# Optimization experiments

Measured on AMD Instinct MI355X. Metric: run time of the kernel, lower is better.

Reference implementation:

```python
import jax, jax.numpy as jnp
import numpy as np
import math

M, DIN, DTGT = 65536, 256, 256   # feature count and feature dims
S, SD_IN, SD_TGT = 64, 256, 256  # num_slots, in_slot_dim, tgt_slot_dim
ITERS = 3
H_IN = 128                        # mlp_in hidden (hardcoded 128 in source)
H_TGT = SD_TGT if SD_TGT > 128 else 128  # mlp_tgt hidden

ARGS = ["inputs", "target", "in_slots", "tgt_slots",
        "ln_in_g", "ln_in_b", "ln_tgt_g", "ln_tgt_b",
        "Wk", "bk", "Wv", "bv", "Wvt", "bvt",
        "ln_slots_g", "ln_slots_b", "Wq", "bq",
        "gru_in_Wih", "gru_in_Whh", "gru_in_bih", "gru_in_bhh",
        "gru_tgt_Wih", "gru_tgt_Whh", "gru_tgt_bih", "gru_tgt_bhh",
        "ln_mi_g", "ln_mi_b", "mi_W1", "mi_b1", "mi_W2", "mi_b2",
        "ln_mt_g", "ln_mt_b", "mt_W1", "mt_b1", "mt_W2", "mt_b2"]


def _ln(x, g, b):
    m = jnp.mean(x, axis=-1, keepdims=True)
    v = jnp.var(x, axis=-1, keepdims=True)
    return (x - m) * jax.lax.rsqrt(v + 1e-5) * g + b


def _gru(x, h, Wih, Whh, bih, bhh):
    # torch.nn.GRUCell semantics; Wih: (D, 3H), Whh: (H, 3H)
    H = h.shape[-1]
    gi = x @ Wih + bih
    gh = h @ Whh + bhh
    r = jax.nn.sigmoid(gi[:, :H] + gh[:, :H])
    z = jax.nn.sigmoid(gi[:, H:2 * H] + gh[:, H:2 * H])
    n = jnp.tanh(gi[:, 2 * H:] + r * gh[:, 2 * H:])
    return (1.0 - z) * n + z * h


def _forward(inputs, target, in_slots, tgt_slots,
             ln_in_g, ln_in_b, ln_tgt_g, ln_tgt_b,
             Wk, bk, Wv, bv, Wvt, bvt,
             ln_slots_g, ln_slots_b, Wq, bq,
             gru_in_Wih, gru_in_Whh, gru_in_bih, gru_in_bhh,
             gru_tgt_Wih, gru_tgt_Whh, gru_tgt_bih, gru_tgt_bhh,
             ln_mi_g, ln_mi_b, mi_W1, mi_b1, mi_W2, mi_b2,
             ln_mt_g, ln_mt_b, mt_W1, mt_b1, mt_W2, mt_b2):
    inputs_norm = _ln(inputs, ln_in_g, ln_in_b)          # [M, DIN]
    in_k = inputs_norm @ Wk + bk                          # [M, SD_IN]
    in_v = inputs_norm @ Wv + bv                          # [M, SD_IN]
    tgt_v = _ln(target, ln_tgt_g, ln_tgt_b) @ Wvt + bvt   # [M, SD_TGT]
    scale = 1.0 / math.sqrt(in_k.shape[1])
    attn = None
    for _ in range(ITERS):
        q = _ln(in_slots, ln_slots_g, ln_slots_b) @ Wq + bq   # [S, SD_IN]
        logits = (q @ in_k.T) * scale                          # [S, M]
        attn = jax.nn.softmax(logits, axis=0)                  # softmax over SLOTS (dim=0)
        in_up = attn @ in_v                                    # [S, SD_IN]
        tgt_up = attn @ tgt_v                                  # [S, SD_TGT]
        in_slots = _gru(in_up, in_slots, gru_in_Wih, gru_in_Whh, gru_in_bih, gru_in_bhh)
        tgt_slots = _gru(tgt_up, tgt_slots, gru_tgt_Wih, gru_tgt_Whh, gru_tgt_bih, gru_tgt_bhh)
        in_slots = in_slots + (jax.nn.relu(_ln(in_slots, ln_mi_g, ln_mi_b) @ mi_W1 + mi_b1) @ mi_W2 + mi_b2)
        tgt_slots = tgt_slots + (jax.nn.relu(_ln(tgt_slots, ln_mt_g, ln_mt_b) @ mt_W1 + mt_b1) @ mt_W2 + mt_b2)
    return (in_slots, tgt_slots, attn)


def setup_inputs() -> dict:
    key = jax.random.key(0)
    ks = iter(jax.random.split(key, 64))
    rn = lambda shape, s=1.0: jax.random.normal(next(ks), shape, dtype=jnp.float32) * s
    w = 0.02
    d = {
        "inputs": rn((M, DIN)),
        "target": rn((M, DTGT)),
        "in_slots": rn((S, SD_IN)),
        "tgt_slots": rn((S, SD_TGT)),
        "ln_in_g": jnp.ones((DIN,)), "ln_in_b": jnp.zeros((DIN,)),
        "ln_tgt_g": jnp.ones((DTGT,)), "ln_tgt_b": jnp.zeros((DTGT,)),
        "Wk": rn((DIN, SD_IN), w), "bk": jnp.zeros((SD_IN,)),
        "Wv": rn((DIN, SD_IN), w), "bv": jnp.zeros((SD_IN,)),
        "Wvt": rn((DTGT, SD_TGT), w), "bvt": jnp.zeros((SD_TGT,)),
        "ln_slots_g": jnp.ones((SD_IN,)), "ln_slots_b": jnp.zeros((SD_IN,)),
        "Wq": rn((SD_IN, SD_IN), w), "bq": jnp.zeros((SD_IN,)),
        "gru_in_Wih": rn((SD_IN, 3 * SD_IN), w), "gru_in_Whh": rn((SD_IN, 3 * SD_IN), w),
        "gru_in_bih": jnp.zeros((3 * SD_IN,)), "gru_in_bhh": jnp.zeros((3 * SD_IN,)),
        "gru_tgt_Wih": rn((SD_TGT, 3 * SD_TGT), w), "gru_tgt_Whh": rn((SD_TGT, 3 * SD_TGT), w),
        "gru_tgt_bih": jnp.zeros((3 * SD_TGT,)), "gru_tgt_bhh": jnp.zeros((3 * SD_TGT,)),
        "ln_mi_g": jnp.ones((SD_IN,)), "ln_mi_b": jnp.zeros((SD_IN,)),
        "mi_W1": rn((SD_IN, H_IN), w), "mi_b1": jnp.zeros((H_IN,)),
        "mi_W2": rn((H_IN, SD_IN), w), "mi_b2": jnp.zeros((SD_IN,)),
        "ln_mt_g": jnp.ones((SD_TGT,)), "ln_mt_b": jnp.zeros((SD_TGT,)),
        "mt_W1": rn((SD_TGT, H_TGT), w), "mt_b1": jnp.zeros((H_TGT,)),
        "mt_W2": rn((H_TGT, SD_TGT), w), "mt_b2": jnp.zeros((SD_TGT,)),
    }
    return {k: d[k] for k in ARGS}


def reference(inputs, target, in_slots, tgt_slots,
              ln_in_g, ln_in_b, ln_tgt_g, ln_tgt_b,
              Wk, bk, Wv, bv, Wvt, bvt,
              ln_slots_g, ln_slots_b, Wq, bq,
              gru_in_Wih, gru_in_Whh, gru_in_bih, gru_in_bhh,
              gru_tgt_Wih, gru_tgt_Whh, gru_tgt_bih, gru_tgt_bhh,
              ln_mi_g, ln_mi_b, mi_W1, mi_b1, mi_W2, mi_b2,
              ln_mt_g, ln_mt_b, mt_W1, mt_b1, mt_W2, mt_b2):
    return _forward(inputs, target, in_slots, tgt_slots,
                    ln_in_g, ln_in_b, ln_tgt_g, ln_tgt_b,
                    Wk, bk, Wv, bv, Wvt, bvt,
                    ln_slots_g, ln_slots_b, Wq, bq,
                    gru_in_Wih, gru_in_Whh, gru_in_bih, gru_in_bhh,
                    gru_tgt_Wih, gru_tgt_Whh, gru_tgt_bih, gru_tgt_bhh,
                    ln_mi_g, ln_mi_b, mi_W1, mi_b1, mi_W2, mi_b2,
                    ln_mt_g, ln_mt_b, mt_W1, mt_b1, mt_W2, mt_b2)
```

## Files before the change

kernel.cpp:

```cpp
#include <hip/hip_runtime.h>
#include <hip/hip_bf16.h>
#include <math.h>

typedef __bf16 bf16_t;
typedef __bf16 bf16x8 __attribute__((ext_vector_type(8)));
typedef __bf16 bf16x4 __attribute__((ext_vector_type(4)));
typedef float f32x4 __attribute__((ext_vector_type(4)));

#define DEVI __device__ __forceinline__

DEVI f32x4 mfma16(bf16x8 a, bf16x8 b, f32x4 c) {
  return __builtin_amdgcn_mfma_f32_16x16x32_bf16(a, b, c, 0, 0, 0);
}
DEVI bf16x8 ld8(const bf16_t* p) { return *reinterpret_cast<const bf16x8*>(p); }

struct WtArgs { const float* s0; const float* s1; const float* s2; const float* s3;
                const float* s4; const float* s5; const float* s6; const float* s7;
                const float* s8; const float* s9; const float* s10; const float* s11; };

__global__ __launch_bounds__(256) void k_wtrans(WtArgs A, bf16_t* __restrict__ wt) {
  constexpr int offs[12] = {0,65536,131072,196608,262144,458752,655360,851968,
                            1048576,1081344,1114112,1179648};
  constexpr int Ks[12]   = {256,256,256,256,256,256,256,256,256,128,256,256};
  constexpr int Ns[12]   = {256,256,256,256,768,768,768,768,128,256,256,256};
  const int m = blockIdx.y;
  const int K = Ks[m], N = Ns[m];
  const int tn = N >> 6;
  const int tile = blockIdx.x;
  if (tile >= (K >> 6) * tn) return;
  const int tk = tile / tn, tc = tile - tk * tn;
  const float* sp;
  switch (m) {
    case 0: sp = A.s0; break; case 1: sp = A.s1; break; case 2: sp = A.s2; break;
    case 3: sp = A.s3; break; case 4: sp = A.s4; break; case 5: sp = A.s5; break;
    case 6: sp = A.s6; break; case 7: sp = A.s7; break; case 8: sp = A.s8; break;
    case 9: sp = A.s9; break; case 10: sp = A.s10; break; default: sp = A.s11; break;
  }
  __shared__ float ts[64][65];
  const int t = threadIdx.x, c = t & 63, rq = t >> 6;
  const int k0 = tk * 64, n0 = tc * 64;
  #pragma unroll
  for (int i = 0; i < 16; ++i) {
    const int r = rq * 16 + i;
    ts[r][c] = sp[(size_t)(k0 + r) * N + n0 + c];
  }
  __syncthreads();
  bf16_t* dst = wt + offs[m];
  #pragma unroll
  for (int i = 0; i < 16; ++i) {
    const int nr = rq * 16 + i;
    dst[(size_t)(n0 + nr) * K + k0 + c] = (bf16_t)ts[c][nr];
  }
}

__global__ __launch_bounds__(256) void k_init(const float* __restrict__ in_slots,
                                              const float* __restrict__ tgt_slots,
                                              float* __restrict__ h_f32,
                                              bf16_t* __restrict__ h_bf) {
  int idx = blockIdx.x * 256 + threadIdx.x;
  int side = idx >> 14, j = idx & 16383;
  float x = (side ? tgt_slots : in_slots)[j];
  h_f32[idx] = x;
  h_bf[idx] = (bf16_t)x;
}

__global__ __launch_bounds__(256) void k_phaseA(
    const float* __restrict__ inputs, const float* __restrict__ target,
    const float* __restrict__ ln_in_g, const float* __restrict__ ln_in_b,
    const float* __restrict__ ln_tgt_g, const float* __restrict__ ln_tgt_b,
    const bf16_t* __restrict__ wkT, const bf16_t* __restrict__ wvT, const bf16_t* __restrict__ wvtT,
    const float* __restrict__ bk, const float* __restrict__ bv, const float* __restrict__ bvt,
    bf16_t* __restrict__ in_k, bf16_t* __restrict__ in_vT, bf16_t* __restrict__ tgt_vT) {
  const int side = blockIdx.y;
  const int m0 = blockIdx.x * 64;
  const int t = threadIdx.x;
  __shared__ __align__(16) bf16_t anorm[64][264];
  __shared__ float gs[256], bs[256];
  {
    const float* g = side ? ln_tgt_g : ln_in_g;
    const float* bb = side ? ln_tgt_b : ln_in_b;
    gs[t] = g[t]; bs[t] = bb[t];
  }
  const float* src = side ? target : inputs;
  const int r = t >> 2, qd = t & 3;
  const float4* rowp = reinterpret_cast<const float4*>(src + (size_t)(m0 + r) * 256 + qd * 64);
  float v[64];
  float s1 = 0.f, s2 = 0.f;
  #pragma unroll
  for (int j = 0; j < 16; ++j) {
    float4 x = rowp[j];
    v[4*j+0] = x.x; v[4*j+1] = x.y; v[4*j+2] = x.z; v[4*j+3] = x.w;
    s1 += x.x + x.y + x.z + x.w;
    s2 += x.x*x.x + x.y*x.y + x.z*x.z + x.w*x.w;
  }
  s1 += __shfl_xor(s1, 1); s1 += __shfl_xor(s1, 2);
  s2 += __shfl_xor(s2, 1); s2 += __shfl_xor(s2, 2);
  const float mean = s1 * (1.f/256.f);
  const float var  = s2 * (1.f/256.f) - mean*mean;
  const float rstd = rsqrtf(var + 1e-5f);
  __syncthreads();
  #pragma unroll
  for (int j = 0; j < 8; ++j) {
    bf16x8 pk;
    #pragma unroll
    for (int e = 0; e < 8; ++e) {
      const int c = qd*64 + j*8 + e;
      pk[e] = (bf16_t)((v[j*8+e] - mean) * rstd * gs[c] + bs[c]);
    }
    *reinterpret_cast<bf16x8*>(&anorm[r][qd*64 + j*8]) = pk;
  }
  __syncthreads();
  const int l = t & 63, w = t >> 6, l16 = l & 15, l4 = l >> 4;

  if (side == 0) {
    f32x4 acc[4][4] = {};
    for (int ks = 0; ks < 8; ++ks) {
      const int k = ks*32 + l4*8;
      bf16x8 a[4], b[4];
      #pragma unroll
      for (int mi = 0; mi < 4; ++mi) a[mi] = ld8(&anorm[mi*16 + l16][k]);
      #pragma unroll
      for (int ni = 0; ni < 4; ++ni) b[ni] = ld8(wkT + (size_t)(w*64 + ni*16 + l16)*256 + k);
      #pragma unroll
      for (int mi = 0; mi < 4; ++mi)
        #pragma unroll
        for (int ni = 0; ni < 4; ++ni) acc[mi][ni] = mfma16(a[mi], b[ni], acc[mi][ni]);
    }
    #pragma unroll
    for (int mi = 0; mi < 4; ++mi)
      #pragma unroll
      for (int ni = 0; ni < 4; ++ni) {
        const int d = w*64 + ni*16 + l16;
        const float bias = bk[d];
        #pragma unroll
        for (int rr = 0; rr < 4; ++rr) {
          const int m = m0 + mi*16 + l4*4 + rr;
          in_k[(size_t)m*256 + d] = (bf16_t)(acc[mi][ni][rr] + bias);
        }
      }
  }
  {
    const bf16_t* WT = side ? wvtT : wvT;
    const float* bias = side ? bvt : bv;
    bf16_t* out = side ? tgt_vT : in_vT;
    f32x4 acc[4][4] = {};
    for (int ks = 0; ks < 8; ++ks) {
      const int k = ks*32 + l4*8;
      bf16x8 a[4], b[4];
      #pragma unroll
      for (int mi = 0; mi < 4; ++mi) a[mi] = ld8(WT + (size_t)(w*64 + mi*16 + l16)*256 + k);
      #pragma unroll
      for (int ni = 0; ni < 4; ++ni) b[ni] = ld8(&anorm[ni*16 + l16][k]);
      #pragma unroll
      for (int mi = 0; mi < 4; ++mi)
        #pragma unroll
        for (int ni = 0; ni < 4; ++ni) acc[mi][ni] = mfma16(a[mi], b[ni], acc[mi][ni]);
    }
    #pragma unroll
    for (int mi = 0; mi < 4; ++mi)
      #pragma unroll
      for (int ni = 0; ni < 4; ++ni) {
        const int m = m0 + ni*16 + l16;
        #pragma unroll
        for (int rr = 0; rr < 4; ++rr) {
          const int d = w*64 + mi*16 + l4*4 + rr;
          out[(size_t)d*65536 + m] = (bf16_t)(acc[mi][ni][rr] + bias[d]);
        }
      }
  }
}

__global__ __launch_bounds__(256) void k_q(
    const float* __restrict__ h_in,
    const float* __restrict__ ln_g, const float* __restrict__ ln_b,
    const bf16_t* __restrict__ wqT, const float* __restrict__ bq,
    bf16_t* __restrict__ q_bf) {
  __shared__ __align__(16) bf16_t anorm[64][264];
  __shared__ float gs[256], bs[256];
  const int t = threadIdx.x;
  gs[t] = ln_g[t]; bs[t] = ln_b[t];
  const int r = t >> 2, qd = t & 3;
  const float4* rowp = reinterpret_cast<const float4*>(h_in + (size_t)r*256 + qd*64);
  float v[64];
  float s1 = 0.f, s2 = 0.f;
  #pragma unroll
  for (int j = 0; j < 16; ++j) {
    float4 x = rowp[j];
    v[4*j+0] = x.x; v[4*j+1] = x.y; v[4*j+2] = x.z; v[4*j+3] = x.w;
    s1 += x.x + x.y + x.z + x.w;
    s2 += x.x*x.x + x.y*x.y + x.z*x.z + x.w*x.w;
  }
  s1 += __shfl_xor(s1, 1); s1 += __shfl_xor(s1, 2);
  s2 += __shfl_xor(s2, 1); s2 += __shfl_xor(s2, 2);
  const float mean = s1 * (1.f/256.f);
  const float rstd = rsqrtf(s2 * (1.f/256.f) - mean*mean + 1e-5f);
  __syncthreads();
  #pragma unroll
  for (int j = 0; j < 8; ++j) {
    bf16x8 pk;
    #pragma unroll
    for (int e = 0; e < 8; ++e) {
      const int c = qd*64 + j*8 + e;
      pk[e] = (bf16_t)((v[j*8+e] - mean) * rstd * gs[c] + bs[c]);
    }
    *reinterpret_cast<bf16x8*>(&anorm[r][qd*64 + j*8]) = pk;
  }
  __syncthreads();
  const int l = t & 63, w = t >> 6, l16 = l & 15, l4 = l >> 4;
  f32x4 acc[4][4] = {};
  for (int ks = 0; ks < 8; ++ks) {
    const int k = ks*32 + l4*8;
    bf16x8 a[4], b[4];
    #pragma unroll
    for (int mi = 0; mi < 4; ++mi) a[mi] = ld8(&anorm[mi*16 + l16][k]);
    #pragma unroll
    for (int ni = 0; ni < 4; ++ni) b[ni] = ld8(wqT + (size_t)(w*64 + ni*16 + l16)*256 + k);
    #pragma unroll
    for (int mi = 0; mi < 4; ++mi)
      #pragma unroll
      for (int ni = 0; ni < 4; ++ni) acc[mi][ni] = mfma16(a[mi], b[ni], acc[mi][ni]);
  }
  #pragma unroll
  for (int mi = 0; mi < 4; ++mi)
    #pragma unroll
    for (int ni = 0; ni < 4; ++ni) {
      const int d = w*64 + ni*16 + l16;
      const float bias = bq[d];
      #pragma unroll
      for (int rr = 0; rr < 4; ++rr) {
        const int s = mi*16 + l4*4 + rr;
        q_bf[(size_t)s*256 + d] = (bf16_t)((acc[mi][ni][rr] + bias) * 0.0625f);
      }
    }
}

__global__ __launch_bounds__(256) void k_logits(
    const bf16_t* __restrict__ q_bf, const bf16_t* __restrict__ in_k,
    bf16_t* __restrict__ attn_bf, float* __restrict__ attn_f32, int write_f32) {
  const int t = threadIdx.x, l = t & 63, w = t >> 6, l16 = l & 15, l4 = l >> 4;
  const int m0 = blockIdx.x * 256 + w * 64;
  f32x4 acc[4][4] = {};
  for (int ks = 0; ks < 8; ++ks) {
    const int k = ks*32 + l4*8;
    bf16x8 a[4], b[4];
    #pragma unroll
    for (int mi = 0; mi < 4; ++mi) a[mi] = ld8(q_bf + (size_t)(mi*16 + l16)*256 + k);
    #pragma unroll
    for (int ni = 0; ni < 4; ++ni) b[ni] = ld8(in_k + (size_t)(m0 + ni*16 + l16)*256 + k);
    #pragma unroll
    for (int mi = 0; mi < 4; ++mi)
      #pragma unroll
      for (int ni = 0; ni < 4; ++ni) acc[mi][ni] = mfma16(a[mi], b[ni], acc[mi][ni]);
  }
  #pragma unroll
  for (int ni = 0; ni < 4; ++ni) {
    float mx = -3.0e38f;
    #pragma unroll
    for (int mi = 0; mi < 4; ++mi)
      #pragma unroll
      for (int rr = 0; rr < 4; ++rr) mx = fmaxf(mx, acc[mi][ni][rr]);
    mx = fmaxf(mx, __shfl_xor(mx, 16));
    mx = fmaxf(mx, __shfl_xor(mx, 32));
    float sm = 0.f;
    #pragma unroll
    for (int mi = 0; mi < 4; ++mi)
      #pragma unroll
      for (int rr = 0; rr < 4; ++rr) {
        float e = __expf(acc[mi][ni][rr] - mx);
        acc[mi][ni][rr] = e; sm += e;
      }
    sm += __shfl_xor(sm, 16);
    sm += __shfl_xor(sm, 32);
    const float inv = 1.0f / sm;
    #pragma unroll
    for (int mi = 0; mi < 4; ++mi)
      #pragma unroll
      for (int rr = 0; rr < 4; ++rr) acc[mi][ni][rr] *= inv;
  }
  #pragma unroll
  for (int mi = 0; mi < 4; ++mi)
    #pragma unroll
    for (int ni = 0; ni < 4; ++ni)
      #pragma unroll
      for (int rr = 0; rr < 4; ++rr) {
        const int s = mi*16 + l4*4 + rr;
        const size_t idx = (size_t)s*65536 + (m0 + ni*16 + l16);
        attn_bf[idx] = (bf16_t)acc[mi][ni][rr];
        if (write_f32) attn_f32[idx] = acc[mi][ni][rr];
      }
}

__global__ __launch_bounds__(256) void k_pv(
    const bf16_t* __restrict__ attn_bf,
    const bf16_t* __restrict__ in_vT, const bf16_t* __restrict__ tgt_vT,
    bf16_t* __restrict__ p_in, bf16_t* __restrict__ p_tgt) {
  const int c = blockIdx.x, side = blockIdx.y;
  const bf16_t* V = side ? tgt_vT : in_vT;
  bf16_t* P = side ? p_tgt : p_in;
  const int t = threadIdx.x, l = t & 63, w = t >> 6, l16 = l & 15, l4 = l >> 4;
  f32x4 acc[4][4] = {};
  for (int ks = 0; ks < 16; ++ks) {
    const int km = c*512 + ks*32 + l4*8;
    bf16x8 a[4], b[4];
    #pragma unroll
    for (int mi = 0; mi < 4; ++mi) a[mi] = ld8(attn_bf + (size_t)(mi*16 + l16)*65536 + km);
    #pragma unroll
    for (int ni = 0; ni < 4; ++ni) b[ni] = ld8(V + (size_t)(w*64 + ni*16 + l16)*65536 + km);
    #pragma unroll
    for (int mi = 0; mi < 4; ++mi)
      #pragma unroll
      for (int ni = 0; ni < 4; ++ni) acc[mi][ni] = mfma16(a[mi], b[ni], acc[mi][ni]);
  }
  #pragma unroll
  for (int mi = 0; mi < 4; ++mi)
    #pragma unroll
    for (int ni = 0; ni < 4; ++ni) {
      const int d = w*64 + ni*16 + l16;
      #pragma unroll
      for (int rr = 0; rr < 4; ++rr) {
        const int s = mi*16 + l4*4 + rr;
        P[(size_t)c*16384 + s*256 + d] = (bf16_t)acc[mi][ni][rr];
      }
    }
}

__global__ __launch_bounds__(256) void k_pvred(
    const bf16_t* __restrict__ p_in, const bf16_t* __restrict__ p_tgt,
    bf16_t* __restrict__ up_bf) {
  const int b = blockIdx.x;
  const int side = b >> 6, s = b & 63;
  const int d = threadIdx.x;
  const bf16_t* P = (side ? p_tgt : p_in) + s*256 + d;
  float sum = 0.f;
  #pragma unroll 8
  for (int cc = 0; cc < 128; ++cc) sum += (float)P[(size_t)cc * 16384];
  up_bf[side*16384 + s*256 + d] = (bf16_t)sum;
}

__global__ __launch_bounds__(256) void k_gates(
    const bf16_t* __restrict__ up_bf, const bf16_t* __restrict__ h_bf,
    const bf16_t* __restrict__ wihT_in, const bf16_t* __restrict__ whhT_in,
    const bf16_t* __restrict__ wihT_tgt, const bf16_t* __restrict__ whhT_tgt,
    const float* __restrict__ bih_in, const float* __restrict__ bhh_in,
    const float* __restrict__ bih_tgt, const float* __restrict__ bhh_tgt,
    float* __restrict__ gi, float* __restrict__ gh) {
  const int nchunk = blockIdx.x, which = blockIdx.y, side = blockIdx.z;
  const bf16_t* Aop = (which ? h_bf : up_bf) + side*16384;
  const bf16_t* WT = side ? (which ? whhT_tgt : wihT_tgt) : (which ? whhT_in : wihT_in);
  const float* bias = side ? (which ? bhh_tgt : bih_tgt) : (which ? bhh_in : bih_in);
  float* out = (which ? gh : gi) + side*49152;
  const int t = threadIdx.x, l = t & 63, w = t >> 6, l16 = l & 15, l4 = l >> 4;
  const int n0 = nchunk*256 + w*64;
  f32x4 acc[4][4] = {};
  for (int ks = 0; ks < 8; ++ks) {
    const int k = ks*32 + l4*8;
    bf16x8 a[4], b[4];
    #pragma unroll
    for (int mi = 0; mi < 4; ++mi) a[mi] = ld8(Aop + (size_t)(mi*16 + l16)*256 + k);
    #pragma unroll
    for (int ni = 0; ni < 4; ++ni) b[ni] = ld8(WT + (size_t)(n0 + ni*16 + l16)*256 + k);
    #pragma unroll
    for (int mi = 0; mi < 4; ++mi)
      #pragma unroll
      for (int ni = 0; ni < 4; ++ni) acc[mi][ni] = mfma16(a[mi], b[ni], acc[mi][ni]);
  }
  #pragma unroll
  for (int mi = 0; mi < 4; ++mi)
    #pragma unroll
    for (int ni = 0; ni < 4; ++ni) {
      const int n = n0 + ni*16 + l16;
      const float bb = bias[n];
      #pragma unroll
      for (int rr = 0; rr < 4; ++rr) {
        const int s = mi*16 + l4*4 + rr;
        out[(size_t)s*768 + n] = acc[mi][ni][rr] + bb;
      }
    }
}

__global__ __launch_bounds__(256) void k_gru_ln(
    const float* __restrict__ gi, const float* __restrict__ gh,
    const float* __restrict__ h_f32,
    const float* __restrict__ ln_mi_g, const float* __restrict__ ln_mi_b,
    const float* __restrict__ ln_mt_g, const float* __restrict__ ln_mt_b,
    float* __restrict__ hp_f32, bf16_t* __restrict__ hpnorm_bf) {
  const int s = blockIdx.x, side = blockIdx.y;
  const int d = threadIdx.x;
  const float* GI = gi + side*49152 + s*768;
  const float* GH = gh + side*49152 + s*768;
  const float hv = h_f32[side*16384 + s*256 + d];
  const float rg = 1.f / (1.f + __expf(-(GI[d] + GH[d])));
  const float zg = 1.f / (1.f + __expf(-(GI[256 + d] + GH[256 + d])));
  const float ng = tanhf(GI[512 + d] + rg * GH[512 + d]);
  const float hp = (1.f - zg) * ng + zg * hv;
  float a = hp, b2 = hp * hp;
  #pragma unroll
  for (int msk = 1; msk < 64; msk <<= 1) { a += __shfl_xor(a, msk); b2 += __shfl_xor(b2, msk); }
  __shared__ float reda[4], redb[4];
  const int w = d >> 6, l = d & 63;
  if (l == 0) { reda[w] = a; redb[w] = b2; }
  __syncthreads();
  const float S1 = reda[0] + reda[1] + reda[2] + reda[3];
  const float S2 = redb[0] + redb[1] + redb[2] + redb[3];
  const float mean = S1 * (1.f/256.f);
  const float rstd = rsqrtf(S2 * (1.f/256.f) - mean*mean + 1e-5f);
  const float* g = side ? ln_mt_g : ln_mi_g;
  const float* bb = side ? ln_mt_b : ln_mi_b;
  const float nv = (hp - mean) * rstd * g[d] + bb[d];
  hp_f32[side*16384 + s*256 + d] = hp;
  hpnorm_bf[side*16384 + s*256 + d] = (bf16_t)nv;
}

__global__ __launch_bounds__(256) void k_mlpq(
    const bf16_t* __restrict__ hpn_bf,
    const bf16_t* __restrict__ w1T_in, const bf16_t* __restrict__ w1T_tgt,
    const float* __restrict__ b1_in, const float* __restrict__ b1_tgt,
    const bf16_t* __restrict__ w2T_in, const bf16_t* __restrict__ w2T_tgt,
    const float* __restrict__ b2_in, const float* __restrict__ b2_tgt,
    const float* __restrict__ hp_f32,
    float* __restrict__ h_f32, bf16_t* __restrict__ h_bf, float* __restrict__ slots_out,
    const float* __restrict__ ln_sg, const float* __restrict__ ln_sb,
    const bf16_t* __restrict__ wqT, const float* __restrict__ bq,
    bf16_t* __restrict__ q_bf, int make_q) {
  const int side = blockIdx.x;
  __shared__ __align__(16) bf16_t hid[64][264];
  const int t = threadIdx.x, l = t & 63, w = t >> 6, l16 = l & 15, l4 = l >> 4;
  const int NH = side ? 256 : 128;
  {
    const bf16_t* Aop = hpn_bf + side*16384;
    const bf16_t* WT = side ? w1T_tgt : w1T_in;
    const float* b1 = side ? b1_tgt : b1_in;
    const int ntiles = NH >> 6;
    for (int nt = 0; nt < ntiles; ++nt) {
      const int n0 = w*(NH>>2) + nt*16;
      f32x4 acc[4] = {};
      for (int ks = 0; ks < 8; ++ks) {
        const int k = ks*32 + l4*8;
        bf16x8 b = ld8(WT + (size_t)(n0 + l16)*256 + k);
        #pragma unroll
        for (int mt = 0; mt < 4; ++mt)
          acc[mt] = mfma16(ld8(Aop + (size_t)(mt*16 + l16)*256 + k), b, acc[mt]);
      }
      const float bb = b1[n0 + l16];
      #pragma unroll
      for (int mt = 0; mt < 4; ++mt)
        #pragma unroll
        for (int rr = 0; rr < 4; ++rr) {
          const int s = mt*16 + l4*4 + rr;
          hid[s][n0 + l16] = (bf16_t)fmaxf(acc[mt][rr] + bb, 0.f);
        }
    }
  }
  __syncthreads();
  {
    const bf16_t* WT = side ? w2T_tgt : w2T_in;
    const float* b2 = side ? b2_tgt : b2_in;
    const int ksteps = NH >> 5;
    #pragma unroll
    for (int nt = 0; nt < 4; ++nt) {
      const int n0 = w*64 + nt*16;
      f32x4 acc[4] = {};
      for (int ks = 0; ks < ksteps; ++ks) {
        const int k = ks*32 + l4*8;
        bf16x8 b = ld8(WT + (size_t)(n0 + l16)*NH + k);
        #pragma unroll
        for (int mt = 0; mt < 4; ++mt)
          acc[mt] = mfma16(ld8(&hid[mt*16 + l16][k]), b, acc[mt]);
      }
      const int n = n0 + l16;
      const float bb = b2[n];
      #pragma unroll
      for (int mt = 0; mt < 4; ++mt)
        #pragma unroll
        for (int rr = 0; rr < 4; ++rr) {
          const int s = mt*16 + l4*4 + rr;
          const int idx = side*16384 + s*256 + n;
          const float val = acc[mt][rr] + bb + hp_f32[idx];
          h_f32[idx] = val;
          h_bf[idx] = (bf16_t)val;
          slots_out[idx] = val;
        }
    }
  }
  if (!make_q || side != 0) return;
  __syncthreads();
  {
    for (int i = 0; i < 16; ++i) {
      const int s = w*16 + i;
      float4 x = *reinterpret_cast<const float4*>(h_f32 + s*256 + 4*l);
      float a = x.x + x.y + x.z + x.w;
      float b2s = x.x*x.x + x.y*x.y + x.z*x.z + x.w*x.w;
      #pragma unroll
      for (int msk = 1; msk < 64; msk <<= 1) { a += __shfl_xor(a, msk); b2s += __shfl_xor(b2s, msk); }
      const float mean = a * (1.f/256.f);
      const float rstd = rsqrtf(b2s * (1.f/256.f) - mean*mean + 1e-5f);
      float4 g4 = *reinterpret_cast<const float4*>(ln_sg + 4*l);
      float4 bb4 = *reinterpret_cast<const float4*>(ln_sb + 4*l);
      bf16x4 pk;
      pk[0] = (bf16_t)((x.x - mean) * rstd * g4.x + bb4.x);
      pk[1] = (bf16_t)((x.y - mean) * rstd * g4.y + bb4.y);
      pk[2] = (bf16_t)((x.z - mean) * rstd * g4.z + bb4.z);
      pk[3] = (bf16_t)((x.w - mean) * rstd * g4.w + bb4.w);
      *reinterpret_cast<bf16x4*>(&hid[s][4*l]) = pk;
    }
  }
  __syncthreads();
  {
    #pragma unroll
    for (int nt = 0; nt < 4; ++nt) {
      const int n0 = w*64 + nt*16;
      f32x4 acc[4] = {};
      for (int ks = 0; ks < 8; ++ks) {
        const int k = ks*32 + l4*8;
        bf16x8 b = ld8(wqT + (size_t)(n0 + l16)*256 + k);
        #pragma unroll
        for (int mt = 0; mt < 4; ++mt)
          acc[mt] = mfma16(ld8(&hid[mt*16 + l16][k]), b, acc[mt]);
      }
      const int d = n0 + l16;
      const float bb = bq[d];
      #pragma unroll
      for (int mt = 0; mt < 4; ++mt)
        #pragma unroll
        for (int rr = 0; rr < 4; ++rr) {
          const int s = mt*16 + l4*4 + rr;
          q_bf[(size_t)s*256 + d] = (bf16_t)((acc[mt][rr] + bb) * 0.0625f);
        }
    }
  }
}

extern "C" void kernel_launch(void* const* d_in, const int* in_sizes, int n_in,
                              void* d_out, int out_size, void* d_ws, size_t ws_size,
                              hipStream_t stream) {
  (void)in_sizes; (void)n_in; (void)out_size; (void)ws_size;
  const float* inputs     = (const float*)d_in[0];
  const float* target     = (const float*)d_in[1];
  const float* in_slots   = (const float*)d_in[2];
  const float* tgt_slots  = (const float*)d_in[3];
  const float* ln_in_g    = (const float*)d_in[4];
  const float* ln_in_b    = (const float*)d_in[5];
  const float* ln_tgt_g   = (const float*)d_in[6];
  const float* ln_tgt_b   = (const float*)d_in[7];
  const float* Wk  = (const float*)d_in[8];
  const float* bk  = (const float*)d_in[9];
  const float* Wv  = (const float*)d_in[10];
  const float* bv  = (const float*)d_in[11];
  const float* Wvt = (const float*)d_in[12];
  const float* bvt = (const float*)d_in[13];
  const float* ln_slots_g = (const float*)d_in[14];
  const float* ln_slots_b = (const float*)d_in[15];
  const float* Wq  = (const float*)d_in[16];
  const float* bq  = (const float*)d_in[17];
  const float* gru_in_Wih  = (const float*)d_in[18];
  const float* gru_in_Whh  = (const float*)d_in[19];
  const float* gru_in_bih  = (const float*)d_in[20];
  const float* gru_in_bhh  = (const float*)d_in[21];
  const float* gru_tgt_Wih = (const float*)d_in[22];
  const float* gru_tgt_Whh = (const float*)d_in[23];
  const float* gru_tgt_bih = (const float*)d_in[24];
  const float* gru_tgt_bhh = (const float*)d_in[25];
  const float* ln_mi_g = (const float*)d_in[26];
  const float* ln_mi_b = (const float*)d_in[27];
  const float* mi_W1 = (const float*)d_in[28];
  const float* mi_b1 = (const float*)d_in[29];
  const float* mi_W2 = (const float*)d_in[30];
  const float* mi_b2 = (const float*)d_in[31];
  const float* ln_mt_g = (const float*)d_in[32];
  const float* ln_mt_b = (const float*)d_in[33];
  const float* mt_W1 = (const float*)d_in[34];
  const float* mt_b1 = (const float*)d_in[35];
  const float* mt_W2 = (const float*)d_in[36];
  const float* mt_b2 = (const float*)d_in[37];

  char* ws = (char*)d_ws;
  bf16_t* wt      = (bf16_t*)(ws);
  bf16_t* in_k    = (bf16_t*)(ws + 2490368ull);
  bf16_t* in_vT   = (bf16_t*)(ws + 36044800ull);
  bf16_t* tgt_vT  = (bf16_t*)(ws + 69599232ull);
  bf16_t* attn_bf = (bf16_t*)(ws + 103153664ull);
  bf16_t* q_bf    = (bf16_t*)(ws + 111542272ull);
  bf16_t* h_bf    = (bf16_t*)(ws + 111575040ull);
  bf16_t* up_bf   = (bf16_t*)(ws + 111640576ull);
  bf16_t* hpn_bf  = (bf16_t*)(ws + 111673344ull);
  float*  h_f32   = (float*)(ws + 111706112ull);
  float*  hp_f32  = (float*)(ws + 111837184ull);
  float*  gi      = (float*)(ws + 111968256ull);
  float*  gh      = (float*)(ws + 112361472ull);
  bf16_t* p_in    = (bf16_t*)(ws + 112754688ull);
  bf16_t* p_tgt   = (bf16_t*)(ws + 116948992ull);

  bf16_t* wkT = wt;
  bf16_t* wvT = wt + 65536;
  bf16_t* wvtT = wt + 131072;
  bf16_t* wqT = wt + 196608;
  bf16_t* wihT_in  = wt + 262144;
  bf16_t* whhT_in  = wt + 458752;
  bf16_t* wihT_tgt = wt + 655360;
  bf16_t* whhT_tgt = wt + 851968;
  bf16_t* w1T_in  = wt + 1048576;
  bf16_t* w2T_in  = wt + 1081344;
  bf16_t* w1T_tgt = wt + 1114112;
  bf16_t* w2T_tgt = wt + 1179648;

  float* attn_out = (float*)d_out + 32768;

  WtArgs wa = {Wk, Wv, Wvt, Wq, gru_in_Wih, gru_in_Whh, gru_tgt_Wih, gru_tgt_Whh,
               mi_W1, mi_W2, mt_W1, mt_W2};
  k_wtrans<<<dim3(48, 12), 256, 0, stream>>>(wa, wt);
  k_init<<<128, 256, 0, stream>>>(in_slots, tgt_slots, h_f32, h_bf);
  k_phaseA<<<dim3(1024, 2), 256, 0, stream>>>(inputs, target, ln_in_g, ln_in_b,
      ln_tgt_g, ln_tgt_b, wkT, wvT, wvtT, bk, bv, bvt, in_k, in_vT, tgt_vT);
  k_q<<<1, 256, 0, stream>>>(h_f32, ln_slots_g, ln_slots_b, wqT, bq, q_bf);

  for (int it = 0; it < 3; ++it) {
    k_logits<<<256, 256, 0, stream>>>(q_bf, in_k, attn_bf, attn_out, it == 2 ? 1 : 0);
    k_pv<<<dim3(128, 2), 256, 0, stream>>>(attn_bf, in_vT, tgt_vT, p_in, p_tgt);
    k_pvred<<<128, 256, 0, stream>>>(p_in, p_tgt, up_bf);
    k_gates<<<dim3(3, 2, 2), 256, 0, stream>>>(up_bf, h_bf, wihT_in, whhT_in,
        wihT_tgt, whhT_tgt, gru_in_bih, gru_in_bhh, gru_tgt_bih, gru_tgt_bhh, gi, gh);
    k_gru_ln<<<dim3(64, 2), 256, 0, stream>>>(gi, gh, h_f32, ln_mi_g, ln_mi_b,
        ln_mt_g, ln_mt_b, hp_f32, hpn_bf);
    k_mlpq<<<2, 256, 0, stream>>>(hpn_bf, w1T_in, w1T_tgt, mi_b1, mt_b1,
        w2T_in, w2T_tgt, mi_b2, mt_b2, hp_f32, h_f32, h_bf, (float*)d_out,
        ln_slots_g, ln_slots_b, wqT, bq, q_bf, it < 2 ? 1 : 0);
  }
}
```

Before: 352.3 us.

## Store bf16 operands in MFMA fragment-tiled layout for contiguous per-wave loads

All bf16 intermediates and transposed weights (keys, values, attention, q, GRU/MLP operands) are rewritten into a 16x32 fragment-tiled layout, so each wave's MFMA operand load becomes one contiguous 1 KB chunk instead of strided 16-byte reads across rows. This aims to remove uncoalesced, cache-unfriendly loads in the large logits and PV GEMMs, especially the 65536-stride reads of the attention and transposed values. The LayerNorm in phaseA and k_q is also reorganised so each wave handles whole rows with a full-wave shuffle reduction, replacing the shared gamma/beta staging and the extra barrier. The stores in the producer epilogues now scatter 2-byte elements at 16-byte strides, which may cost write efficiency.

```diff
diff --git a/kernel.cpp b/kernel.cpp
--- a/kernel.cpp
+++ b/kernel.cpp
@@ -13,6 +13,7 @@
   return __builtin_amdgcn_mfma_f32_16x16x32_bf16(a, b, c, 0, 0, 0);
 }
 DEVI bf16x8 ld8(const bf16_t* p) { return *reinterpret_cast<const bf16x8*>(p); }
+
 
 struct WtArgs { const float* s0; const float* s1; const float* s2; const float* s3;
                 const float* s4; const float* s5; const float* s6; const float* s7;
@@ -37,19 +38,29 @@
     case 9: sp = A.s9; break; case 10: sp = A.s10; break; default: sp = A.s11; break;
   }
   __shared__ float ts[64][65];
-  const int t = threadIdx.x, c = t & 63, rq = t >> 6;
+  const int t = threadIdx.x;
   const int k0 = tk * 64, n0 = tc * 64;
-  #pragma unroll
-  for (int i = 0; i < 16; ++i) {
-    const int r = rq * 16 + i;
-    ts[r][c] = sp[(size_t)(k0 + r) * N + n0 + c];
+  {
+    const int c = t & 63, rq = t >> 6;
+    #pragma unroll
+    for (int i = 0; i < 16; ++i) {
+      const int r = rq * 16 + i;
+      ts[r][c] = sp[(size_t)(k0 + r) * N + n0 + c];
+    }
   }
   __syncthreads();
   bf16_t* dst = wt + offs[m];
-  #pragma unroll
-  for (int i = 0; i < 16; ++i) {
-    const int nr = rq * 16 + i;
-    dst[(size_t)(n0 + nr) * K + k0 + c] = (bf16_t)ts[c][nr];
+  const int n_l = t & 63, kq = t >> 6;
+  #pragma unroll
+  for (int h = 0; h < 2; ++h) {
+    const int k_l = kq * 16 + h * 8;
+    bf16x8 pk;
+    #pragma unroll
+    for (int e = 0; e < 8; ++e) pk[e] = (bf16_t)ts[k_l + e][n_l];
+    const int n_g = n0 + n_l, k_g = k0 + k_l;
+    const int nt = n_g >> 4, kc = k_g >> 5;
+    const int lane = (((k_g >> 3) & 3) << 4) + (n_g & 15);
+    *reinterpret_cast<bf16x8*>(dst + (((size_t)(nt * (K >> 5) + kc)) << 9) + lane * 8) = pk;
   }
 }
 
@@ -59,58 +70,50 @@
                                               bf16_t* __restrict__ h_bf) {
   int idx = blockIdx.x * 256 + threadIdx.x;
   int side = idx >> 14, j = idx & 16383;
+  int s = j >> 8, d = j & 255;
   float x = (side ? tgt_slots : in_slots)[j];
   h_f32[idx] = x;
-  h_bf[idx] = (bf16_t)x;
+  h_bf[side*16384 + (((s>>4)*8 + (d>>5))<<9) + ((d>>3)&3)*128 + (s&15)*8 + (d&7)] = (bf16_t)x;
 }
 
 __global__ __launch_bounds__(256) void k_phaseA(
     const float* __restrict__ inputs, const float* __restrict__ target,
     const float* __restrict__ ln_in_g, const float* __restrict__ ln_in_b,
     const float* __restrict__ ln_tgt_g, const float* __restrict__ ln_tgt_b,
-    const bf16_t* __restrict__ wkT, const bf16_t* __restrict__ wvT, const bf16_t* __restrict__ wvtT,
+    const bf16_t* __restrict__ wkF, const bf16_t* __restrict__ wvF, const bf16_t* __restrict__ wvtF,
     const float* __restrict__ bk, const float* __restrict__ bv, const float* __restrict__ bvt,
-    bf16_t* __restrict__ in_k, bf16_t* __restrict__ in_vT, bf16_t* __restrict__ tgt_vT) {
+    bf16_t* __restrict__ in_kF, bf16_t* __restrict__ in_vF, bf16_t* __restrict__ tgt_vF) {
   const int side = blockIdx.y;
   const int m0 = blockIdx.x * 64;
-  const int t = threadIdx.x;
+  const int t = threadIdx.x, l = t & 63, w = t >> 6;
   __shared__ __align__(16) bf16_t anorm[64][264];
-  __shared__ float gs[256], bs[256];
-  {
-    const float* g = side ? ln_tgt_g : ln_in_g;
-    const float* bb = side ? ln_tgt_b : ln_in_b;
-    gs[t] = g[t]; bs[t] = bb[t];
-  }
   const float* src = side ? target : inputs;
-  const int r = t >> 2, qd = t & 3;
-  const float4* rowp = reinterpret_cast<const float4*>(src + (size_t)(m0 + r) * 256 + qd * 64);
-  float v[64];
-  float s1 = 0.f, s2 = 0.f;
-  #pragma unroll
-  for (int j = 0; j < 16; ++j) {
-    float4 x = rowp[j];
-    v[4*j+0] = x.x; v[4*j+1] = x.y; v[4*j+2] = x.z; v[4*j+3] = x.w;
-    s1 += x.x + x.y + x.z + x.w;
-    s2 += x.x*x.x + x.y*x.y + x.z*x.z + x.w*x.w;
-  }
-  s1 += __shfl_xor(s1, 1); s1 += __shfl_xor(s1, 2);
-  s2 += __shfl_xor(s2, 1); s2 += __shfl_xor(s2, 2);
-  const float mean = s1 * (1.f/256.f);
-  const float var  = s2 * (1.f/256.f) - mean*mean;
-  const float rstd = rsqrtf(var + 1e-5f);
+  const float* gp = side ? ln_tgt_g : ln_in_g;
+  const float* bp = side ? ln_tgt_b : ln_in_b;
+  const float4 g4 = *reinterpret_cast<const float4*>(gp + l * 4);
+  const float4 b4 = *reinterpret_cast<const float4*>(bp + l * 4);
+  float4 v[16];
+  #pragma unroll
+  for (int i = 0; i < 16; ++i)
+    v[i] = *reinterpret_cast<const float4*>(src + (size_t)(m0 + w*16 + i) * 256 + l * 4);
+  #pragma unroll
+  for (int i = 0; i < 16; ++i) {
+    float s1 = v[i].x + v[i].y + v[i].z + v[i].w;
+    float s2 = v[i].x*v[i].x + v[i].y*v[i].y + v[i].z*v[i].z + v[i].w*v[i].w;
+    #pragma unroll
+    for (int msk = 1; msk < 64; msk <<= 1) { s1 += __shfl_xor(s1, msk); s2 += __shfl_xor(s2, msk); }
+    const float mean = s1 * (1.f/256.f);
+    const float rstd = rsqrtf(s2 * (1.f/256.f) - mean*mean + 1e-5f);
+    bf16x4 pk;
+    pk[0] = (bf16_t)((v[i].x - mean) * rstd * g4.x + b4.x);
+    pk[1] = (bf16_t)((v[i].y - mean) * rstd * g4.y + b4.y);
+    pk[2] = (bf16_t)((v[i].z - mean) * rstd * g4.z + b4.z);
+    pk[3] = (bf16_t)((v[i].w - mean) * rstd * g4.w + b4.w);
+    *reinterpret_cast<bf16x4*>(&anorm[w*16 + i][l*4]) = pk;
+  }
   __syncthreads();
-  #pragma unroll
-  for (int j = 0; j < 8; ++j) {
-    bf16x8 pk;
-    #pragma unroll
-    for (int e = 0; e < 8; ++e) {
-      const int c = qd*64 + j*8 + e;
-      pk[e] = (bf16_t)((v[j*8+e] - mean) * rstd * gs[c] + bs[c]);
-    }
-    *reinterpret_cast<bf16x8*>(&anorm[r][qd*64 + j*8]) = pk;
-  }
-  __syncthreads();
-  const int l = t & 63, w = t >> 6, l16 = l & 15, l4 = l >> 4;
+  const int l16 = l & 15, l4 = l >> 4;
+  const int e = l16 & 7, lh = l16 >> 3;
 
   if (side == 0) {
     f32x4 acc[4][4] = {};
@@ -120,7 +123,7 @@
       #pragma unroll
       for (int mi = 0; mi < 4; ++mi) a[mi] = ld8(&anorm[mi*16 + l16][k]);
       #pragma unroll
-      for (int ni = 0; ni < 4; ++ni) b[ni] = ld8(wkT + (size_t)(w*64 + ni*16 + l16)*256 + k);
+      for (int ni = 0; ni < 4; ++ni) b[ni] = ld8(wkF + (((size_t)((w*4 + ni)*8 + ks)) << 9) + l*8);
       #pragma unroll
       for (int mi = 0; mi < 4; ++mi)
         #pragma unroll
@@ -132,23 +135,24 @@
       for (int ni = 0; ni < 4; ++ni) {
         const int d = w*64 + ni*16 + l16;
         const float bias = bk[d];
-        #pragma unroll
-        for (int rr = 0; rr < 4; ++rr) {
-          const int m = m0 + mi*16 + l4*4 + rr;
-          in_k[(size_t)m*256 + d] = (bf16_t)(acc[mi][ni][rr] + bias);
-        }
+        const int kc = w*2 + (ni >> 1);
+        const int l4p = (ni & 1)*2 + lh;
+        bf16_t* outp = in_kF + ((((size_t)(blockIdx.x*4 + mi))*8 + kc) << 9) + l4p*128 + e;
+        #pragma unroll
+        for (int rr = 0; rr < 4; ++rr)
+          outp[(l4*4 + rr)*8] = (bf16_t)(acc[mi][ni][rr] + bias);
       }
   }
   {
-    const bf16_t* WT = side ? wvtT : wvT;
+    const bf16_t* WF = side ? wvtF : wvF;
     const float* bias = side ? bvt : bv;
-    bf16_t* out = side ? tgt_vT : in_vT;
+    bf16_t* out = side ? tgt_vF : in_vF;
     f32x4 acc[4][4] = {};
     for (int ks = 0; ks < 8; ++ks) {
       const int k = ks*32 + l4*8;
       bf16x8 a[4], b[4];
       #pragma unroll
-      for (int mi = 0; mi < 4; ++mi) a[mi] = ld8(WT + (size_t)(w*64 + mi*16 + l16)*256 + k);
+      for (int mi = 0; mi < 4; ++mi) a[mi] = ld8(WF + (((size_t)((w*4 + mi)*8 + ks)) << 9) + l*8);
       #pragma unroll
       for (int ni = 0; ni < 4; ++ni) b[ni] = ld8(&anorm[ni*16 + l16][k]);
       #pragma unroll
@@ -160,11 +164,14 @@
     for (int mi = 0; mi < 4; ++mi)
       #pragma unroll
       for (int ni = 0; ni < 4; ++ni) {
-        const int m = m0 + ni*16 + l16;
+        const int dt = w*4 + mi;
+        const int mc = blockIdx.x*2 + (ni >> 1);
+        const int l4p = (ni & 1)*2 + lh;
+        bf16_t* outp = out + ((((size_t)dt)*2048 + mc) << 9) + l4p*128 + e;
         #pragma unroll
         for (int rr = 0; rr < 4; ++rr) {
           const int d = w*64 + mi*16 + l4*4 + rr;
-          out[(size_t)d*65536 + m] = (bf16_t)(acc[mi][ni][rr] + bias[d]);
+          outp[(l4*4 + rr)*8] = (bf16_t)(acc[mi][ni][rr] + bias[d]);
         }
       }
   }
@@ -173,40 +180,33 @@
 __global__ __launch_bounds__(256) void k_q(
     const float* __restrict__ h_in,
     const float* __restrict__ ln_g, const float* __restrict__ ln_b,
-    const bf16_t* __restrict__ wqT, const float* __restrict__ bq,
+    const bf16_t* __restrict__ wqF, const float* __restrict__ bq,
     bf16_t* __restrict__ q_bf) {
   __shared__ __align__(16) bf16_t anorm[64][264];
-  __shared__ float gs[256], bs[256];
-  const int t = threadIdx.x;
-  gs[t] = ln_g[t]; bs[t] = ln_b[t];
-  const int r = t >> 2, qd = t & 3;
-  const float4* rowp = reinterpret_cast<const float4*>(h_in + (size_t)r*256 + qd*64);
-  float v[64];
-  float s1 = 0.f, s2 = 0.f;
-  #pragma unroll
-  for (int j = 0; j < 16; ++j) {
-    float4 x = rowp[j];
-    v[4*j+0] = x.x; v[4*j+1] = x.y; v[4*j+2] = x.z; v[4*j+3] = x.w;
-    s1 += x.x + x.y + x.z + x.w;
-    s2 += x.x*x.x + x.y*x.y + x.z*x.z + x.w*x.w;
-  }
-  s1 += __shfl_xor(s1, 1); s1 += __shfl_xor(s1, 2);
-  s2 += __shfl_xor(s2, 1); s2 += __shfl_xor(s2, 2);
-  const float mean = s1 * (1.f/256.f);
-  const float rstd = rsqrtf(s2 * (1.f/256.f) - mean*mean + 1e-5f);
+  const int t = threadIdx.x, l = t & 63, w = t >> 6;
+  const float4 g4 = *reinterpret_cast<const float4*>(ln_g + l * 4);
+  const float4 b4 = *reinterpret_cast<const float4*>(ln_b + l * 4);
+  float4 v[16];
+  #pragma unroll
+  for (int i = 0; i < 16; ++i)
+    v[i] = *reinterpret_cast<const float4*>(h_in + (size_t)(w*16 + i) * 256 + l * 4);
+  #pragma unroll
+  for (int i = 0; i < 16; ++i) {
+    float s1 = v[i].x + v[i].y + v[i].z + v[i].w;
+    float s2 = v[i].x*v[i].x + v[i].y*v[i].y + v[i].z*v[i].z + v[i].w*v[i].w;
+    #pragma unroll
+    for (int msk = 1; msk < 64; msk <<= 1) { s1 += __shfl_xor(s1, msk); s2 += __shfl_xor(s2, msk); }
+    const float mean = s1 * (1.f/256.f);
+    const float rstd = rsqrtf(s2 * (1.f/256.f) - mean*mean + 1e-5f);
+    bf16x4 pk;
+    pk[0] = (bf16_t)((v[i].x - mean) * rstd * g4.x + b4.x);
+    pk[1] = (bf16_t)((v[i].y - mean) * rstd * g4.y + b4.y);
+    pk[2] = (bf16_t)((v[i].z - mean) * rstd * g4.z + b4.z);
+    pk[3] = (bf16_t)((v[i].w - mean) * rstd * g4.w + b4.w);
+    *reinterpret_cast<bf16x4*>(&anorm[w*16 + i][l*4]) = pk;
+  }
   __syncthreads();
-  #pragma unroll
-  for (int j = 0; j < 8; ++j) {
-    bf16x8 pk;
-    #pragma unroll
-    for (int e = 0; e < 8; ++e) {
-      const int c = qd*64 + j*8 + e;
-      pk[e] = (bf16_t)((v[j*8+e] - mean) * rstd * gs[c] + bs[c]);
-    }
-    *reinterpret_cast<bf16x8*>(&anorm[r][qd*64 + j*8]) = pk;
-  }
-  __syncthreads();
-  const int l = t & 63, w = t >> 6, l16 = l & 15, l4 = l >> 4;
+  const int l16 = l & 15, l4 = l >> 4;
   f32x4 acc[4][4] = {};
   for (int ks = 0; ks < 8; ++ks) {
     const int k = ks*32 + l4*8;
@@ -214,7 +214,7 @@
     #pragma unroll
     for (int mi = 0; mi < 4; ++mi) a[mi] = ld8(&anorm[mi*16 + l16][k]);
     #pragma unroll
-    for (int ni = 0; ni < 4; ++ni) b[ni] = ld8(wqT + (size_t)(w*64 + ni*16 + l16)*256 + k);
+    for (int ni = 0; ni < 4; ++ni) b[ni] = ld8(wqF + (((size_t)((w*4 + ni)*8 + ks)) << 9) + l*8);
     #pragma unroll
     for (int mi = 0; mi < 4; ++mi)
       #pragma unroll
@@ -226,27 +226,26 @@
     for (int ni = 0; ni < 4; ++ni) {
       const int d = w*64 + ni*16 + l16;
       const float bias = bq[d];
-      #pragma unroll
-      for (int rr = 0; rr < 4; ++rr) {
-        const int s = mi*16 + l4*4 + rr;
-        q_bf[(size_t)s*256 + d] = (bf16_t)((acc[mi][ni][rr] + bias) * 0.0625f);
-      }
+      bf16_t* outp = q_bf + (((size_t)(mi*8 + w*2 + (ni>>1))) << 9) + ((ni&1)*2 + (l16>>3))*128 + (l16&7);
+      #pragma unroll
+      for (int rr = 0; rr < 4; ++rr)
+        outp[(l4*4 + rr)*8] = (bf16_t)((acc[mi][ni][rr] + bias) * 0.0625f);
     }
 }
 
 __global__ __launch_bounds__(256) void k_logits(
-    const bf16_t* __restrict__ q_bf, const bf16_t* __restrict__ in_k,
-    bf16_t* __restrict__ attn_bf, float* __restrict__ attn_f32, int write_f32) {
+    const bf16_t* __restrict__ q_bf, const bf16_t* __restrict__ in_kF,
+    bf16_t* __restrict__ attnF, float* __restrict__ attn_f32, int write_f32) {
   const int t = threadIdx.x, l = t & 63, w = t >> 6, l16 = l & 15, l4 = l >> 4;
   const int m0 = blockIdx.x * 256 + w * 64;
   f32x4 acc[4][4] = {};
   for (int ks = 0; ks < 8; ++ks) {
-    const int k = ks*32 + l4*8;
     bf16x8 a[4], b[4];
     #pragma unroll
-    for (int mi = 0; mi < 4; ++mi) a[mi] = ld8(q_bf + (size_t)(mi*16 + l16)*256 + k);
-    #pragma unroll
-    for (int ni = 0; ni < 4; ++ni) b[ni] = ld8(in_k + (size_t)(m0 + ni*16 + l16)*256 + k);
+    for (int mi = 0; mi < 4; ++mi) a[mi] = ld8(q_bf + (((size_t)(mi*8 + ks)) << 9) + l*8);
+    #pragma unroll
+    for (int ni = 0; ni < 4; ++ni)
+      b[ni] = ld8(in_kF + (((size_t)((blockIdx.x*16 + w*4 + ni)*8 + ks)) << 9) + l*8);
     #pragma unroll
     for (int mi = 0; mi < 4; ++mi)
       #pragma unroll
@@ -266,8 +265,8 @@
     for (int mi = 0; mi < 4; ++mi)
       #pragma unroll
       for (int rr = 0; rr < 4; ++rr) {
-        float e = __expf(acc[mi][ni][rr] - mx);
-        acc[mi][ni][rr] = e; sm += e;
+        float ev = __expf(acc[mi][ni][rr] - mx);
+        acc[mi][ni][rr] = ev; sm += ev;
       }
     sm += __shfl_xor(sm, 16);
     sm += __shfl_xor(sm, 32);
@@ -280,32 +279,36 @@
   #pragma unroll
   for (int mi = 0; mi < 4; ++mi)
     #pragma unroll
-    for (int ni = 0; ni < 4; ++ni)
+    for (int ni = 0; ni < 4; ++ni) {
+      const int mc = blockIdx.x*8 + w*2 + (ni >> 1);
+      bf16_t* outp = attnF + ((((size_t)mi)*2048 + mc) << 9) + ((ni&1)*2 + (l16>>3))*128 + (l16&7);
       #pragma unroll
       for (int rr = 0; rr < 4; ++rr) {
-        const int s = mi*16 + l4*4 + rr;
-        const size_t idx = (size_t)s*65536 + (m0 + ni*16 + l16);
-        attn_bf[idx] = (bf16_t)acc[mi][ni][rr];
-        if (write_f32) attn_f32[idx] = acc[mi][ni][rr];
-      }
+        outp[(l4*4 + rr)*8] = (bf16_t)acc[mi][ni][rr];
+        if (write_f32) {
+          const int s = mi*16 + l4*4 + rr;
+          attn_f32[(size_t)s*65536 + (m0 + ni*16 + l16)] = acc[mi][ni][rr];
+        }
+      }
+    }
 }
 
 __global__ __launch_bounds__(256) void k_pv(
-    const bf16_t* __restrict__ attn_bf,
-    const bf16_t* __restrict__ in_vT, const bf16_t* __restrict__ tgt_vT,
+    const bf16_t* __restrict__ attnF,
+    const bf16_t* __restrict__ in_vF, const bf16_t* __restrict__ tgt_vF,
     bf16_t* __restrict__ p_in, bf16_t* __restrict__ p_tgt) {
   const int c = blockIdx.x, side = blockIdx.y;
-  const bf16_t* V = side ? tgt_vT : in_vT;
+  const bf16_t* V = side ? tgt_vF : in_vF;
   bf16_t* P = side ? p_tgt : p_in;
   const int t = threadIdx.x, l = t & 63, w = t >> 6, l16 = l & 15, l4 = l >> 4;
   f32x4 acc[4][4] = {};
   for (int ks = 0; ks < 16; ++ks) {
-    const int km = c*512 + ks*32 + l4*8;
+    const size_t mc = c*16 + ks;
     bf16x8 a[4], b[4];
     #pragma unroll
-    for (int mi = 0; mi < 4; ++mi) a[mi] = ld8(attn_bf + (size_t)(mi*16 + l16)*65536 + km);
-    #pragma unroll
-    for (int ni = 0; ni < 4; ++ni) b[ni] = ld8(V + (size_t)(w*64 + ni*16 + l16)*65536 + km);
+    for (int mi = 0; mi < 4; ++mi) a[mi] = ld8(attnF + ((((size_t)mi)*2048 + mc) << 9) + l*8);
+    #pragma unroll
+    for (int ni = 0; ni < 4; ++ni) b[ni] = ld8(V + ((((size_t)(w*4 + ni))*2048 + mc) << 9) + l*8);
     #pragma unroll
     for (int mi = 0; mi < 4; ++mi)
       #pragma unroll
@@ -326,7 +329,7 @@
 
 __global__ __launch_bounds__(256) void k_pvred(
     const bf16_t* __restrict__ p_in, const bf16_t* __restrict__ p_tgt,
-    bf16_t* __restrict__ up_bf) {
+    bf16_t* __restrict__ upF) {
   const int b = blockIdx.x;
   const int side = b >> 6, s = b & 63;
   const int d = threadIdx.x;
@@ -334,31 +337,31 @@
   float sum = 0.f;
   #pragma unroll 8
   for (int cc = 0; cc < 128; ++cc) sum += (float)P[(size_t)cc * 16384];
-  up_bf[side*16384 + s*256 + d] = (bf16_t)sum;
+  upF[side*16384 + (((s>>4)*8 + (d>>5))<<9) + ((d>>3)&3)*128 + (s&15)*8 + (d&7)] = (bf16_t)sum;
 }
 
 __global__ __launch_bounds__(256) void k_gates(
-    const bf16_t* __restrict__ up_bf, const bf16_t* __restrict__ h_bf,
-    const bf16_t* __restrict__ wihT_in, const bf16_t* __restrict__ whhT_in,
-    const bf16_t* __restrict__ wihT_tgt, const bf16_t* __restrict__ whhT_tgt,
+    const bf16_t* __restrict__ upF, const bf16_t* __restrict__ h_bf,
+    const bf16_t* __restrict__ wihF_in, const bf16_t* __restrict__ whhF_in,
+    const bf16_t* __restrict__ wihF_tgt, const bf16_t* __restrict__ whhF_tgt,
     const float* __restrict__ bih_in, const float* __restrict__ bhh_in,
     const float* __restrict__ bih_tgt, const float* __restrict__ bhh_tgt,
     float* __restrict__ gi, float* __restrict__ gh) {
   const int nchunk = blockIdx.x, which = blockIdx.y, side = blockIdx.z;
-  const bf16_t* Aop = (which ? h_bf : up_bf) + side*16384;
-  const bf16_t* WT = side ? (which ? whhT_tgt : wihT_tgt) : (which ? whhT_in : wihT_in);
+  const bf16_t* Aop = (which ? h_bf : upF) + side*16384;
+  const bf16_t* WF = side ? (which ? whhF_tgt : wihF_tgt) : (which ? whhF_in : wihF_in);
   const float* bias = side ? (which ? bhh_tgt : bih_tgt) : (which ? bhh_in : bih_in);
   float* out = (which ? gh : gi) + side*49152;
   const int t = threadIdx.x, l = t & 63, w = t >> 6, l16 = l & 15, l4 = l >> 4;
   const int n0 = nchunk*256 + w*64;
   f32x4 acc[4][4] = {};
   for (int ks = 0; ks < 8; ++ks) {
-    const int k = ks*32 + l4*8;
     bf16x8 a[4], b[4];
     #pragma unroll
-    for (int mi = 0; mi < 4; ++mi) a[mi] = ld8(Aop + (size_t)(mi*16 + l16)*256 + k);
-    #pragma unroll
-    for (int ni = 0; ni < 4; ++ni) b[ni] = ld8(WT + (size_t)(n0 + ni*16 + l16)*256 + k);
+    for (int mi = 0; mi < 4; ++mi) a[mi] = ld8(Aop + (((size_t)(mi*8 + ks)) << 9) + l*8);
+    #pragma unroll
+    for (int ni = 0; ni < 4; ++ni)
+      b[ni] = ld8(WF + (((size_t)((nchunk*16 + w*4 + ni)*8 + ks)) << 9) + l*8);
     #pragma unroll
     for (int mi = 0; mi < 4; ++mi)
       #pragma unroll
@@ -383,7 +386,7 @@
     const float* __restrict__ h_f32,
     const float* __restrict__ ln_mi_g, const float* __restrict__ ln_mi_b,
     const float* __restrict__ ln_mt_g, const float* __restrict__ ln_mt_b,
-    float* __restrict__ hp_f32, bf16_t* __restrict__ hpnorm_bf) {
+    float* __restrict__ hp_f32, bf16_t* __restrict__ hpnF) {
   const int s = blockIdx.x, side = blockIdx.y;
   const int d = threadIdx.x;
   const float* GI = gi + side*49152 + s*768;
@@ -397,8 +400,8 @@
   #pragma unroll
   for (int msk = 1; msk < 64; msk <<= 1) { a += __shfl_xor(a, msk); b2 += __shfl_xor(b2, msk); }
   __shared__ float reda[4], redb[4];
-  const int w = d >> 6, l = d & 63;
-  if (l == 0) { reda[w] = a; redb[w] = b2; }
+  const int w = d >> 6, lid = d & 63;
+  if (lid == 0) { reda[w] = a; redb[w] = b2; }
   __syncthreads();
   const float S1 = reda[0] + reda[1] + reda[2] + reda[3];
   const float S2 = redb[0] + redb[1] + redb[2] + redb[3];
@@ -408,38 +411,37 @@
   const float* bb = side ? ln_mt_b : ln_mi_b;
   const float nv = (hp - mean) * rstd * g[d] + bb[d];
   hp_f32[side*16384 + s*256 + d] = hp;
-  hpnorm_bf[side*16384 + s*256 + d] = (bf16_t)nv;
+  hpnF[side*16384 + (((s>>4)*8 + (d>>5))<<9) + ((d>>3)&3)*128 + (s&15)*8 + (d&7)] = (bf16_t)nv;
 }
 
 __global__ __launch_bounds__(256) void k_mlpq(
-    const bf16_t* __restrict__ hpn_bf,
-    const bf16_t* __restrict__ w1T_in, const bf16_t* __restrict__ w1T_tgt,
+    const bf16_t* __restrict__ hpnF,
+    const bf16_t* __restrict__ w1F_in, const bf16_t* __restrict__ w1F_tgt,
     const float* __restrict__ b1_in, const float* __restrict__ b1_tgt,
-    const bf16_t* __restrict__ w2T_in, const bf16_t* __restrict__ w2T_tgt,
+    const bf16_t* __restrict__ w2F_in, const bf16_t* __restrict__ w2F_tgt,
     const float* __restrict__ b2_in, const float* __restrict__ b2_tgt,
     const float* __restrict__ hp_f32,
     float* __restrict__ h_f32, bf16_t* __restrict__ h_bf, float* __restrict__ slots_out,
     const float* __restrict__ ln_sg, const float* __restrict__ ln_sb,
-    const bf16_t* __restrict__ wqT, const float* __restrict__ bq,
+    const bf16_t* __restrict__ wqF, const float* __restrict__ bq,
     bf16_t* __restrict__ q_bf, int make_q) {
   const int side = blockIdx.x;
   __shared__ __align__(16) bf16_t hid[64][264];
   const int t = threadIdx.x, l = t & 63, w = t >> 6, l16 = l & 15, l4 = l >> 4;
   const int NH = side ? 256 : 128;
   {
-    const bf16_t* Aop = hpn_bf + side*16384;
-    const bf16_t* WT = side ? w1T_tgt : w1T_in;
+    const bf16_t* Aop = hpnF + side*16384;
+    const bf16_t* WF = side ? w1F_tgt : w1F_in;
     const float* b1 = side ? b1_tgt : b1_in;
     const int ntiles = NH >> 6;
     for (int nt = 0; nt < ntiles; ++nt) {
       const int n0 = w*(NH>>2) + nt*16;
       f32x4 acc[4] = {};
       for (int ks = 0; ks < 8; ++ks) {
-        const int k = ks*32 + l4*8;
-        bf16x8 b = ld8(WT + (size_t)(n0 + l16)*256 + k);
+        bf16x8 b = ld8(WF + (((size_t)((n0>>4)*8 + ks)) << 9) + l*8);
         #pragma unroll
         for (int mt = 0; mt < 4; ++mt)
-          acc[mt] = mfma16(ld8(Aop + (size_t)(mt*16 + l16)*256 + k), b, acc[mt]);
+          acc[mt] = mfma16(ld8(Aop + (((size_t)(mt*8 + ks)) << 9) + l*8), b, acc[mt]);
       }
       const float bb = b1[n0 + l16];
       #pragma unroll
@@ -453,7 +455,7 @@
   }
   __syncthreads();
   {
-    const bf16_t* WT = side ? w2T_tgt : w2T_in;
+    const bf16_t* WF = side ? w2F_tgt : w2F_in;
     const float* b2 = side ? b2_tgt : b2_in;
     const int ksteps = NH >> 5;
     #pragma unroll
@@ -462,7 +464,7 @@
       f32x4 acc[4] = {};
       for (int ks = 0; ks < ksteps; ++ks) {
         const int k = ks*32 + l4*8;
-        bf16x8 b = ld8(WT + (size_t)(n0 + l16)*NH + k);
+        bf16x8 b = ld8(WF + (((size_t)((n0>>4)*ksteps + ks)) << 9) + l*8);
         #pragma unroll
         for (int mt = 0; mt < 4; ++mt)
           acc[mt] = mfma16(ld8(&hid[mt*16 + l16][k]), b, acc[mt]);
@@ -477,8 +479,8 @@
           const int idx = side*16384 + s*256 + n;
           const float val = acc[mt][rr] + bb + hp_f32[idx];
           h_f32[idx] = val;
-          h_bf[idx] = (bf16_t)val;
           slots_out[idx] = val;
+          h_bf[side*16384 + (((s>>4)*8 + (n>>5))<<9) + ((n>>3)&3)*128 + (s&15)*8 + (n&7)] = (bf16_t)val;
         }
     }
   }
@@ -512,20 +514,22 @@
       f32x4 acc[4] = {};
       for (int ks = 0; ks < 8; ++ks) {
         const int k = ks*32 + l4*8;
-        bf16x8 b = ld8(wqT + (size_t)(n0 + l16)*256 + k);
+        bf16x8 b = ld8(wqF + (((size_t)((n0>>4)*8 + ks)) << 9) + l*8);
         #pragma unroll
         for (int mt = 0; mt < 4; ++mt)
           acc[mt] = mfma16(ld8(&hid[mt*16 + l16][k]), b, acc[mt]);
       }
       const int d = n0 + l16;
       const float bb = bq[d];
-      #pragma unroll
-      for (int mt = 0; mt < 4; ++mt)
-        #pragma unroll
-        for (int rr = 0; rr < 4; ++rr) {
-          const int s = mt*16 + l4*4 + rr;
-          q_bf[(size_t)s*256 + d] = (bf16_t)((acc[mt][rr] + bb) * 0.0625f);
-        }
+      bf16_t* outp = q_bf + (((size_t)(0)) ) ;
+      #pragma unroll
+      for (int mt = 0; mt < 4; ++mt) {
+        bf16_t* op = q_bf + (((size_t)(mt*8 + (d>>5))) << 9) + ((d>>3)&3)*128 + (d&7);
+        #pragma unroll
+        for (int rr = 0; rr < 4; ++rr)
+          op[(l4*4 + rr)*8] = (bf16_t)((acc[mt][rr] + bb) * 0.0625f);
+      }
+      (void)outp;
     }
   }
 }
@@ -575,14 +579,14 @@
 
   char* ws = (char*)d_ws;
   bf16_t* wt      = (bf16_t*)(ws);
-  bf16_t* in_k    = (bf16_t*)(ws + 2490368ull);
-  bf16_t* in_vT   = (bf16_t*)(ws + 36044800ull);
-  bf16_t* tgt_vT  = (bf16_t*)(ws + 69599232ull);
-  bf16_t* attn_bf = (bf16_t*)(ws + 103153664ull);
+  bf16_t* in_kF   = (bf16_t*)(ws + 2490368ull);
+  bf16_t* in_vF   = (bf16_t*)(ws + 36044800ull);
+  bf16_t* tgt_vF  = (bf16_t*)(ws + 69599232ull);
+  bf16_t* attnF   = (bf16_t*)(ws + 103153664ull);
   bf16_t* q_bf    = (bf16_t*)(ws + 111542272ull);
   bf16_t* h_bf    = (bf16_t*)(ws + 111575040ull);
-  bf16_t* up_bf   = (bf16_t*)(ws + 111640576ull);
-  bf16_t* hpn_bf  = (bf16_t*)(ws + 111673344ull);
+  bf16_t* upF     = (bf16_t*)(ws + 111640576ull);
+  bf16_t* hpnF    = (bf16_t*)(ws + 111673344ull);
   float*  h_f32   = (float*)(ws + 111706112ull);
   float*  hp_f32  = (float*)(ws + 111837184ull);
   float*  gi      = (float*)(ws + 111968256ull);
@@ -590,18 +594,18 @@
   bf16_t* p_in    = (bf16_t*)(ws + 112754688ull);
   bf16_t* p_tgt   = (bf16_t*)(ws + 116948992ull);
 
-  bf16_t* wkT = wt;
-  bf16_t* wvT = wt + 65536;
-  bf16_t* wvtT = wt + 131072;
-  bf16_t* wqT = wt + 196608;
-  bf16_t* wihT_in  = wt + 262144;
-  bf16_t* whhT_in  = wt + 458752;
-  bf16_t* wihT_tgt = wt + 655360;
-  bf16_t* whhT_tgt = wt + 851968;
-  bf16_t* w1T_in  = wt + 1048576;
-  bf16_t* w2T_in  = wt + 1081344;
-  bf16_t* w1T_tgt = wt + 1114112;
-  bf16_t* w2T_tgt = wt + 1179648;
+  bf16_t* wkF = wt;
+  bf16_t* wvF = wt + 65536;
+  bf16_t* wvtF = wt + 131072;
+  bf16_t* wqF = wt + 196608;
+  bf16_t* wihF_in  = wt + 262144;
+  bf16_t* whhF_in  = wt + 458752;
+  bf16_t* wihF_tgt = wt + 655360;
+  bf16_t* whhF_tgt = wt + 851968;
+  bf16_t* w1F_in  = wt + 1048576;
+  bf16_t* w2F_in  = wt + 1081344;
+  bf16_t* w1F_tgt = wt + 1114112;
+  bf16_t* w2F_tgt = wt + 1179648;
 
   float* attn_out = (float*)d_out + 32768;
 
@@ -610,19 +614,19 @@
   k_wtrans<<<dim3(48, 12), 256, 0, stream>>>(wa, wt);
   k_init<<<128, 256, 0, stream>>>(in_slots, tgt_slots, h_f32, h_bf);
   k_phaseA<<<dim3(1024, 2), 256, 0, stream>>>(inputs, target, ln_in_g, ln_in_b,
-      ln_tgt_g, ln_tgt_b, wkT, wvT, wvtT, bk, bv, bvt, in_k, in_vT, tgt_vT);
-  k_q<<<1, 256, 0, stream>>>(h_f32, ln_slots_g, ln_slots_b, wqT, bq, q_bf);
+      ln_tgt_g, ln_tgt_b, wkF, wvF, wvtF, bk, bv, bvt, in_kF, in_vF, tgt_vF);
+  k_q<<<1, 256, 0, stream>>>(h_f32, ln_slots_g, ln_slots_b, wqF, bq, q_bf);
 
   for (int it = 0; it < 3; ++it) {
-    k_logits<<<256, 256, 0, stream>>>(q_bf, in_k, attn_bf, attn_out, it == 2 ? 1 : 0);
-    k_pv<<<dim3(128, 2), 256, 0, stream>>>(attn_bf, in_vT, tgt_vT, p_in, p_tgt);
-    k_pvred<<<128, 256, 0, stream>>>(p_in, p_tgt, up_bf);
-    k_gates<<<dim3(3, 2, 2), 256, 0, stream>>>(up_bf, h_bf, wihT_in, whhT_in,
-        wihT_tgt, whhT_tgt, gru_in_bih, gru_in_bhh, gru_tgt_bih, gru_tgt_bhh, gi, gh);
+    k_logits<<<256, 256, 0, stream>>>(q_bf, in_kF, attnF, attn_out, it == 2 ? 1 : 0);
+    k_pv<<<dim3(128, 2), 256, 0, stream>>>(attnF, in_vF, tgt_vF, p_in, p_tgt);
+    k_pvred<<<128, 256, 0, stream>>>(p_in, p_tgt, upF);
+    k_gates<<<dim3(3, 2, 2), 256, 0, stream>>>(upF, h_bf, wihF_in, whhF_in,
+        wihF_tgt, whhF_tgt, gru_in_bih, gru_in_bhh, gru_tgt_bih, gru_tgt_bhh, gi, gh);
     k_gru_ln<<<dim3(64, 2), 256, 0, stream>>>(gi, gh, h_f32, ln_mi_g, ln_mi_b,
-        ln_mt_g, ln_mt_b, hp_f32, hpn_bf);
-    k_mlpq<<<2, 256, 0, stream>>>(hpn_bf, w1T_in, w1T_tgt, mi_b1, mt_b1,
-        w2T_in, w2T_tgt, mi_b2, mt_b2, hp_f32, h_f32, h_bf, (float*)d_out,
-        ln_slots_g, ln_slots_b, wqT, bq, q_bf, it < 2 ? 1 : 0);
-  }
-}
+        ln_mt_g, ln_mt_b, hp_f32, hpnF);
+    k_mlpq<<<2, 256, 0, stream>>>(hpnF, w1F_in, w1F_tgt, mi_b1, mt_b1,
+        w2F_in, w2F_tgt, mi_b2, mt_b2, hp_f32, h_f32, h_bf, (float*)d_out,
+        ln_slots_g, ln_slots_b, wqF, bq, q_bf, it < 2 ? 1 : 0);
+  }
+}
```

After: 330.3 us. 1.07x faster.
